# Optimization experiments

Measured on AMD Instinct MI355X. Metric: run time of the kernel, lower is better.

The kernel has to match this reference:

```python
import jax, jax.numpy as jnp
import numpy as np
from itertools import combinations

# Static configuration matching init_kwargs / input_specs
ADD = 3        # max subset size (init arg 'add')
N_COLS = 16    # columns_num = x.shape[1]
BATCH = 262144


def _subset_index_tables(n_cols, add):
    """For each subset size i in [2, min(add, n_cols)], an int array [num_subsets_i, i]
    of column indices, in the same lexicographic order as itertools.combinations
    (identical to the original torch loop order)."""
    tables = []
    for i in range(2, min(add, n_cols) + 1):
        tables.append(np.array(list(combinations(range(n_cols), i)), dtype=np.int32))
    return tables

_IDX_TABLES = _subset_index_tables(N_COLS, ADD)


def setup_inputs() -> dict:
    key = jax.random.key(0)
    x = jax.random.normal(key, (BATCH, N_COLS), dtype=jnp.float32)
    return {"x": x}


def reference(x):
    # Original: for every subset c of columns with 2 <= |c| <= add, append
    # prod(x[:, c], axis=1) to the output, after the original columns.
    outs = [x]
    for idx in _IDX_TABLES:           # idx: [m_i, i]
        # x[:, idx] -> [B, m_i, i]; product over subset members -> [B, m_i]
        outs.append(jnp.prod(x[:, idx], axis=2))
    return jnp.concatenate(outs, axis=1)  # [B, n + sum_i C(n, i)]
```

## Files before the change

kernel.cpp:

```cpp
#include <hip/hip_runtime.h>
#include <cstdint>
#include <cstddef>


#define NCOLS       16
#define NOUT        696
#define F4_PER_ROW  174
#define RPB         64
#define THREADS     256
#define CHUNK       58
#define ROWPAD      65

typedef float vfloat4 __attribute__((ext_vector_type(4)));

struct Tab { uint32_t v[NOUT]; };
static constexpr Tab make_tab() {
    Tab T{};
    int n = 0;
    for (uint32_t c = 0; c < NCOLS; ++c)
        T.v[n++] = c | (16u << 8) | (16u << 16);
    for (uint32_t i = 0; i < NCOLS; ++i)
        for (uint32_t j = i + 1; j < NCOLS; ++j)
            T.v[n++] = i | (j << 8) | (16u << 16);
    for (uint32_t i = 0; i < NCOLS; ++i)
        for (uint32_t j = i + 1; j < NCOLS; ++j)
            for (uint32_t k = j + 1; k < NCOLS; ++k)
                T.v[n++] = i | (j << 8) | (k << 16);
    return T;
}
static constexpr Tab HT = make_tab();

template<int COL>
__device__ __forceinline__ float prod_col(const float (&x)[NCOLS]) {
    constexpr uint32_t t = HT.v[COL];
    constexpr int a = t & 31;
    constexpr int b = (t >> 8) & 31;
    constexpr int c = (t >> 16) & 31;
    float r = x[a];
    if constexpr (b < NCOLS) r *= x[b];
    if constexpr (c < NCOLS) r *= x[c];
    return r;
}

template<int C, int END, int PBASE>
struct Emit {
    static __device__ __forceinline__ void run(const float (&x)[NCOLS],
                                               vfloat4 (&st)[CHUNK][ROWPAD],
                                               int lane) {
        vfloat4 o;
        o.x = prod_col<4 * C + 0>(x);
        o.y = prod_col<4 * C + 1>(x);
        o.z = prod_col<4 * C + 2>(x);
        o.w = prod_col<4 * C + 3>(x);
        st[C - PBASE][lane] = o;
        Emit<C + 1, END, PBASE>::run(x, st, lane);
    }
};
template<int END, int PBASE>
struct Emit<END, END, PBASE> {
    static __device__ __forceinline__ void run(const float (&)[NCOLS],
                                               vfloat4 (&)[CHUNK][ROWPAD], int) {}
};

template<int PBASE>
__device__ __forceinline__ void compute_pass(const float (&x)[NCOLS],
                                             vfloat4 (&st)[CHUNK][ROWPAD],
                                             int w, int lane) {
    if      (w == 0) Emit<PBASE +  0, PBASE + 15, PBASE>::run(x, st, lane);
    else if (w == 1) Emit<PBASE + 15, PBASE + 30, PBASE>::run(x, st, lane);
    else if (w == 2) Emit<PBASE + 30, PBASE + 44, PBASE>::run(x, st, lane);
    else             Emit<PBASE + 44, PBASE + 58, PBASE>::run(x, st, lane);
}

template<int PBASE>
__device__ __forceinline__ void drain_pass(const vfloat4 (&st)[CHUNK][ROWPAD],
                                           vfloat4* __restrict__ outv,
                                           int tid, int rows_left) {
#pragma unroll
    for (int d = 0; d < 14; ++d) {
        const int g  = d * THREADS + tid;
        const int rl = g / CHUNK;
        const int c4 = g - rl * CHUNK;
        if (rl < rows_left)
            __builtin_nontemporal_store(st[c4][rl],
                &outv[(size_t)rl * F4_PER_ROW + PBASE + c4]);
    }
    {
        const int g = 14 * THREADS + tid;
        if (g < CHUNK * RPB) {
            const int rl = g / CHUNK;
            const int c4 = g - rl * CHUNK;
            if (rl < rows_left)
                __builtin_nontemporal_store(st[c4][rl],
                    &outv[(size_t)rl * F4_PER_ROW + PBASE + c4]);
        }
    }
}

__global__ __launch_bounds__(THREADS) void algebraic_expand_kernel(
        const float* __restrict__ xg, float* __restrict__ out, int nrows) {
    __shared__ vfloat4 st[CHUNK][ROWPAD];

    const int tid  = threadIdx.x;
    const int lane = tid & 63;
    const int w    = tid >> 6;
    const int r0   = blockIdx.x * RPB;

    float x[NCOLS];
    {
        const int row = r0 + lane;
        if (row < nrows) {
            const vfloat4* xr = (const vfloat4*)xg + (size_t)row * 4;
            const vfloat4 a = xr[0], b = xr[1], c = xr[2], d = xr[3];
            x[0]  = a.x; x[1]  = a.y; x[2]  = a.z; x[3]  = a.w;
            x[4]  = b.x; x[5]  = b.y; x[6]  = b.z; x[7]  = b.w;
            x[8]  = c.x; x[9]  = c.y; x[10] = c.z; x[11] = c.w;
            x[12] = d.x; x[13] = d.y; x[14] = d.z; x[15] = d.w;
        } else {
#pragma unroll
            for (int i = 0; i < NCOLS; ++i) x[i] = 0.0f;
        }
    }

    vfloat4* outv = (vfloat4*)out + (size_t)r0 * F4_PER_ROW;
    const int rem = nrows - r0;
    const int rows_left = rem < RPB ? rem : RPB;

    compute_pass<0>(x, st, w, lane);
    __syncthreads();
    drain_pass<0>(st, outv, tid, rows_left);
    __syncthreads();

    compute_pass<CHUNK>(x, st, w, lane);
    __syncthreads();
    drain_pass<CHUNK>(st, outv, tid, rows_left);
    __syncthreads();

    compute_pass<2 * CHUNK>(x, st, w, lane);
    __syncthreads();
    drain_pass<2 * CHUNK>(st, outv, tid, rows_left);
}

extern "C" void kernel_launch(void* const* d_in, const int* in_sizes, int n_in,
                              void* d_out, int out_size, void* d_ws, size_t ws_size,
                              hipStream_t stream) {
    const float* x = (const float*)d_in[0];
    float* out = (float*)d_out;
    const int nrows = in_sizes[0] / NCOLS;
    const int blocks = (nrows + RPB - 1) / RPB;
    algebraic_expand_kernel<<<blocks, THREADS, 0, stream>>>(x, out, nrows);
}
```

Measured before the change: 780.6 us.

## Use single-wavefront blocks with wave-local LDS staging and no barriers

Each block becomes a single 64-thread wavefront handling 64 rows. It computes and drains 12-float4 column chunks through a small LDS tile, using s_waitcnt instead of __syncthreads. A fast path skips the bounds checks for full blocks, and the stores go back to regular instead of nontemporal. The aim is to remove block-wide barriers and raise occupancy through the much smaller LDS footprint. The trade-off is more passes per row block and losing the nontemporal hint on a large streaming write.

```diff
diff --git a/kernel.cpp b/kernel.cpp
--- a/kernel.cpp
+++ b/kernel.cpp
@@ -6,9 +6,8 @@
 #define NCOLS       16
 #define NOUT        696
 #define F4_PER_ROW  174
-#define RPB         64
-#define THREADS     256
-#define CHUNK       58
+#define THREADS     64
+#define CHUNK       12
 #define ROWPAD      65
 
 typedef float vfloat4 __attribute__((ext_vector_type(4)));
@@ -62,49 +61,46 @@
                                                vfloat4 (&)[CHUNK][ROWPAD], int) {}
 };
 
-template<int PBASE>
-__device__ __forceinline__ void compute_pass(const float (&x)[NCOLS],
-                                             vfloat4 (&st)[CHUNK][ROWPAD],
-                                             int w, int lane) {
-    if      (w == 0) Emit<PBASE +  0, PBASE + 15, PBASE>::run(x, st, lane);
-    else if (w == 1) Emit<PBASE + 15, PBASE + 30, PBASE>::run(x, st, lane);
-    else if (w == 2) Emit<PBASE + 30, PBASE + 44, PBASE>::run(x, st, lane);
-    else             Emit<PBASE + 44, PBASE + 58, PBASE>::run(x, st, lane);
+template<int PBASE, int NC, bool FULL>
+__device__ __forceinline__ void do_pass(const float (&x)[NCOLS],
+                                        vfloat4 (&st)[CHUNK][ROWPAD],
+                                        vfloat4* __restrict__ outv,
+                                        int lane, int rows_left) {
+    Emit<PBASE, PBASE + NC, PBASE>::run(x, st, lane);
+    asm volatile("s_waitcnt lgkmcnt(0)" ::: "memory");
+#pragma unroll
+    for (int i = 0; i < NC; ++i) {
+        const int g  = i * THREADS + lane;
+        const int rl = g / NC;
+        const int c4 = g - rl * NC;
+        const vfloat4 v = st[c4][rl];
+        if (FULL || rl < rows_left)
+            outv[(size_t)rl * F4_PER_ROW + PBASE + c4] = v;
+    }
+    asm volatile("s_waitcnt lgkmcnt(0)" ::: "memory");
 }
 
-template<int PBASE>
-__device__ __forceinline__ void drain_pass(const vfloat4 (&st)[CHUNK][ROWPAD],
-                                           vfloat4* __restrict__ outv,
-                                           int tid, int rows_left) {
-#pragma unroll
-    for (int d = 0; d < 14; ++d) {
-        const int g  = d * THREADS + tid;
-        const int rl = g / CHUNK;
-        const int c4 = g - rl * CHUNK;
-        if (rl < rows_left)
-            __builtin_nontemporal_store(st[c4][rl],
-                &outv[(size_t)rl * F4_PER_ROW + PBASE + c4]);
+template<int P, bool FULL>
+struct Passes {
+    static __device__ __forceinline__ void run(const float (&x)[NCOLS],
+                                               vfloat4 (&st)[CHUNK][ROWPAD],
+                                               vfloat4* __restrict__ outv,
+                                               int lane, int rows_left) {
+        constexpr int PBASE = P * CHUNK;
+        constexpr int NC =
+            (PBASE + CHUNK <= F4_PER_ROW) ? CHUNK : (F4_PER_ROW - PBASE);
+        do_pass<PBASE, NC, FULL>(x, st, outv, lane, rows_left);
+        if constexpr (PBASE + NC < F4_PER_ROW)
+            Passes<P + 1, FULL>::run(x, st, outv, lane, rows_left);
     }
-    {
-        const int g = 14 * THREADS + tid;
-        if (g < CHUNK * RPB) {
-            const int rl = g / CHUNK;
-            const int c4 = g - rl * CHUNK;
-            if (rl < rows_left)
-                __builtin_nontemporal_store(st[c4][rl],
-                    &outv[(size_t)rl * F4_PER_ROW + PBASE + c4]);
-        }
-    }
-}
+};
 
 __global__ __launch_bounds__(THREADS) void algebraic_expand_kernel(
         const float* __restrict__ xg, float* __restrict__ out, int nrows) {
     __shared__ vfloat4 st[CHUNK][ROWPAD];
 
-    const int tid  = threadIdx.x;
-    const int lane = tid & 63;
-    const int w    = tid >> 6;
-    const int r0   = blockIdx.x * RPB;
+    const int lane = threadIdx.x;
+    const int r0   = blockIdx.x * THREADS;
 
     float x[NCOLS];
     {
@@ -124,21 +120,13 @@
 
     vfloat4* outv = (vfloat4*)out + (size_t)r0 * F4_PER_ROW;
     const int rem = nrows - r0;
-    const int rows_left = rem < RPB ? rem : RPB;
+    const int rows_left = rem < THREADS ? rem : THREADS;
 
-    compute_pass<0>(x, st, w, lane);
-    __syncthreads();
-    drain_pass<0>(st, outv, tid, rows_left);
-    __syncthreads();
-
-    compute_pass<CHUNK>(x, st, w, lane);
-    __syncthreads();
-    drain_pass<CHUNK>(st, outv, tid, rows_left);
-    __syncthreads();
-
-    compute_pass<2 * CHUNK>(x, st, w, lane);
-    __syncthreads();
-    drain_pass<2 * CHUNK>(st, outv, tid, rows_left);
+    if (rows_left == THREADS) {
+        Passes<0, true>::run(x, st, outv, lane, rows_left);
+    } else {
+        Passes<0, false>::run(x, st, outv, lane, rows_left);
+    }
 }
 
 extern "C" void kernel_launch(void* const* d_in, const int* in_sizes, int n_in,
@@ -147,6 +135,6 @@
     const float* x = (const float*)d_in[0];
     float* out = (float*)d_out;
     const int nrows = in_sizes[0] / NCOLS;
-    const int blocks = (nrows + RPB - 1) / RPB;
+    const int blocks = (nrows + THREADS - 1) / THREADS;
     algebraic_expand_kernel<<<blocks, THREADS, 0, stream>>>(x, out, nrows);
 }
```

Result: slower. 855.8 us (+9.6%).
